# Kernel tuning notes

Hardware: AMD Instinct MI355X
Metric: run time of the kernel (lower is better)

The kernel has to match this reference:

```python
import jax, jax.numpy as jnp
import numpy as np
import math
from jax import lax

B, HID, HD, TD = 16384, 4096, 256, 64
IN_DIM = HID + 6 + TD
NL = 4
SOURCE_SCALE = 0.1


def hat(w):
    z = jnp.zeros_like(w[..., 0])
    wx, wy, wz = w[..., 0], w[..., 1], w[..., 2]
    return jnp.stack([
        jnp.stack([z, -wz, wy], -1),
        jnp.stack([wz, z, -wx], -1),
        jnp.stack([-wy, wx, z], -1)], -2)


def exp_se3(xi):
    # xi: [B,6] = (omega, v); returns [B,4,4]
    w, v = xi[:, :3], xi[:, 3:]
    th = jnp.sqrt(jnp.sum(w * w, -1) + 1e-20)[:, None, None]
    th2 = th * th
    small = th < 1e-3
    ths = jnp.where(small, 1.0, th)
    A = jnp.where(small, 1.0 - th2 / 6.0, jnp.sin(ths) / ths)
    Bc = jnp.where(small, 0.5 - th2 / 24.0, (1.0 - jnp.cos(ths)) / (ths * ths))
    Cc = jnp.where(small, 1.0 / 6.0 - th2 / 120.0, (ths - jnp.sin(ths)) / (ths ** 3))
    W = hat(w)
    W2 = W @ W
    I = jnp.eye(3, dtype=xi.dtype)
    R = I + A * W + Bc * W2
    V = I + Bc * W + Cc * W2
    t = jnp.einsum('bij,bj->bi', V, v)
    top = jnp.concatenate([R, t[:, :, None]], -1)
    bot = jnp.broadcast_to(jnp.array([0.0, 0.0, 0.0, 1.0], xi.dtype), (xi.shape[0], 1, 4))
    return jnp.concatenate([top, bot], -2)


def log_se3(X):
    # X: [B,4,4] -> xi: [B,6]
    R = X[:, :3, :3]
    p = X[:, :3, 3]
    tr = R[:, 0, 0] + R[:, 1, 1] + R[:, 2, 2]
    c = jnp.clip((tr - 1.0) * 0.5, -1.0 + 1e-7, 1.0 - 1e-7)
    th = jnp.arccos(c)[:, None, None]
    small = th < 1e-3
    ths = jnp.where(small, 1.0, th)
    fac = jnp.where(small, 0.5 + th * th / 12.0, ths / (2.0 * jnp.sin(ths)))
    wvee = jnp.stack([R[:, 2, 1] - R[:, 1, 2], R[:, 0, 2] - R[:, 2, 0], R[:, 1, 0] - R[:, 0, 1]], -1)
    w = fac[:, :, 0] * wvee
    W = hat(w)
    W2 = W @ W
    D = jnp.where(small, 1.0 / 12.0, (1.0 - ths * jnp.sin(ths) / (2.0 * (1.0 - jnp.cos(ths)))) / (ths * ths))
    I = jnp.eye(3, dtype=X.dtype)
    Vinv = I - 0.5 * W + D * W2
    v = jnp.einsum('bij,bj->bi', Vinv, p)
    return jnp.concatenate([w, v], -1)


def time_embed(t):
    # t: [B,1] -> [B,TD]
    half = TD // 2
    freqs = jnp.exp(jnp.arange(half, dtype=t.dtype) * (-math.log(10000.0) / (half - 1)))
    e = t * freqs[None, :]
    return jnp.concatenate([jnp.sin(e), jnp.cos(e)], -1)


def layernorm(x, g, b):
    m = jnp.mean(x, -1, keepdims=True)
    var = jnp.mean((x - m) ** 2, -1, keepdims=True)
    return (x - m) * lax.rsqrt(var + 1e-5) * g + b


def setup_inputs() -> dict:
    key = jax.random.key(0)
    ks = jax.random.split(key, 10)
    def lin(k, i, o):
        return jax.random.normal(k, (i, o), jnp.float32) / np.float32(np.sqrt(i))
    return {
        'h': jax.random.normal(ks[0], (B, HID), jnp.float32),
        'xi0': jax.random.normal(ks[1], (B, 6), jnp.float32),
        'W0': lin(ks[2], IN_DIM, HD),
        'b0': jnp.zeros((HD,), jnp.float32),
        'g0': jnp.ones((HD,), jnp.float32),
        'be0': jnp.zeros((HD,), jnp.float32),
        'Wr': jax.random.normal(ks[3], (NL - 1, HD, HD), jnp.float32) / np.float32(np.sqrt(HD)),
        'br': jnp.zeros((NL - 1, HD), jnp.float32),
        'gr': jnp.ones((NL - 1, HD), jnp.float32),
        'ber': jnp.zeros((NL - 1, HD), jnp.float32),
        'Wout': 0.05 * jax.random.normal(ks[4], (HD, 6), jnp.float32),
        'bout': jnp.zeros((6,), jnp.float32),
        'gW1': lin(ks[5], HID, 64),
        'gb1': jnp.zeros((64,), jnp.float32),
        'gW2': lin(ks[6], 64, 1),
        'gb2': jnp.zeros((1,), jnp.float32),
        'n_steps': 10,
    }


def reference(h, xi0, W0, b0, g0, be0, Wr, br, gr, ber, Wout, bout, gW1, gb1, gW2, gb2, n_steps):
    dt = 1.0 / n_steps
    X0 = exp_se3(SOURCE_SCALE * xi0)

    def mlp(x):
        y = layernorm(jax.nn.gelu(x @ W0 + b0, approximate=False), g0, be0)
        for i in range(Wr.shape[0]):
            y = layernorm(jax.nn.gelu(y @ Wr[i] + br[i], approximate=False), gr[i], ber[i])
        return y @ Wout + bout

    def step(X_t, tval):
        xi_t = log_se3(X_t)
        temb = time_embed(jnp.ones((X_t.shape[0], 1), X_t.dtype) * tval)
        v = mlp(jnp.concatenate([h, xi_t, temb], -1))
        X_next = jnp.einsum('bij,bjk->bik', X_t, exp_se3(dt * v))
        return X_next, None

    ts = jnp.arange(n_steps, dtype=h.dtype) * dt
    X1, _ = lax.scan(step, X0, ts)
    gripper = jax.nn.sigmoid(jax.nn.gelu(h @ gW1 + gb1, approximate=False) @ gW2 + gb2)
    return X1, gripper
```

## Files before the change

### kernel.cpp

```cpp
#include <hip/hip_runtime.h>
#include <math.h>

typedef __attribute__((ext_vector_type(8))) __bf16 bf16_8;
typedef __attribute__((ext_vector_type(4))) float f32x4;

#define WS_HPROJ 0
#define WS_BT    16777216
#define WS_WRT   19398656
#define WS_CT    19791872

__device__ __forceinline__ float gelu_f(float x) {
    return 0.5f * x * (1.0f + erff(0.70710678118654752440f * x));
}

__device__ __forceinline__ void exp_se3_dev(const float xi[6], float R[9], float t[3]) {
    float wx = xi[0], wy = xi[1], wz = xi[2];
    float vx = xi[3], vy = xi[4], vz = xi[5];
    float ww = wx*wx + wy*wy + wz*wz;
    float th2 = ww + 1e-20f;
    float th = sqrtf(th2);
    float A, Bc, Cc;
    if (th < 1e-3f) {
        A = 1.f - th2*(1.f/6.f);
        Bc = 0.5f - th2*(1.f/24.f);
        Cc = (1.f/6.f) - th2*(1.f/120.f);
    } else {
        float s = sinf(th), c = cosf(th);
        A = s/th;
        Bc = (1.f - c)/th2;
        Cc = (th - s)/(th2*th);
    }
    float W2[9] = { wx*wx - ww, wx*wy,       wx*wz,
                    wy*wx,      wy*wy - ww,  wy*wz,
                    wz*wx,      wz*wy,       wz*wz - ww };
    R[0] = 1.f + Bc*W2[0];  R[1] = -A*wz + Bc*W2[1]; R[2] =  A*wy + Bc*W2[2];
    R[3] =  A*wz + Bc*W2[3]; R[4] = 1.f + Bc*W2[4];  R[5] = -A*wx + Bc*W2[5];
    R[6] = -A*wy + Bc*W2[6]; R[7] =  A*wx + Bc*W2[7]; R[8] = 1.f + Bc*W2[8];
    float V[9];
    V[0] = 1.f + Cc*W2[0];   V[1] = -Bc*wz + Cc*W2[1]; V[2] =  Bc*wy + Cc*W2[2];
    V[3] =  Bc*wz + Cc*W2[3]; V[4] = 1.f + Cc*W2[4];   V[5] = -Bc*wx + Cc*W2[5];
    V[6] = -Bc*wy + Cc*W2[6]; V[7] =  Bc*wx + Cc*W2[7]; V[8] = 1.f + Cc*W2[8];
    t[0] = V[0]*vx + V[1]*vy + V[2]*vz;
    t[1] = V[3]*vx + V[4]*vy + V[5]*vz;
    t[2] = V[6]*vx + V[7]*vy + V[8]*vz;
}

__device__ __forceinline__ void log_se3_dev(const float R[9], const float p[3], float xi[6]) {
    float tr = R[0] + R[4] + R[8];
    float c = 0.5f*(tr - 1.f);
    c = fminf(fmaxf(c, -1.f + 1e-7f), 1.f - 1e-7f);
    float th = acosf(c);
    float fac, D;
    if (th < 1e-3f) {
        fac = 0.5f + th*th*(1.f/12.f);
        D = 1.f/12.f;
    } else {
        float s = sinf(th), co = cosf(th);
        fac = th/(2.f*s);
        D = (1.f - th*s/(2.f*(1.f - co)))/(th*th);
    }
    float wx = fac*(R[7] - R[5]);
    float wy = fac*(R[2] - R[6]);
    float wz = fac*(R[3] - R[1]);
    float ww = wx*wx + wy*wy + wz*wz;
    float W2[9] = { wx*wx - ww, wx*wy,       wx*wz,
                    wy*wx,      wy*wy - ww,  wy*wz,
                    wz*wx,      wz*wy,       wz*wz - ww };
    float Vi[9];
    Vi[0] = 1.f + D*W2[0];    Vi[1] =  0.5f*wz + D*W2[1]; Vi[2] = -0.5f*wy + D*W2[2];
    Vi[3] = -0.5f*wz + D*W2[3]; Vi[4] = 1.f + D*W2[4];    Vi[5] =  0.5f*wx + D*W2[5];
    Vi[6] =  0.5f*wy + D*W2[6]; Vi[7] = -0.5f*wx + D*W2[7]; Vi[8] = 1.f + D*W2[8];
    xi[0] = wx; xi[1] = wy; xi[2] = wz;
    xi[3] = Vi[0]*p[0] + Vi[1]*p[1] + Vi[2]*p[2];
    xi[4] = Vi[3]*p[0] + Vi[4]*p[1] + Vi[5]*p[2];
    xi[5] = Vi[6]*p[0] + Vi[7]*p[1] + Vi[8]*p[2];
}

__global__ void prep_frag(const float* __restrict__ W0, const float* __restrict__ gW1,
                          const float* __restrict__ Wr, __bf16* __restrict__ BT2,
                          __bf16* __restrict__ WrT2) {
    const int tid = threadIdx.x;
    const int l = tid & 63, q = l >> 4, ln = l & 15;
    if (blockIdx.x < 640) {
        const int t = blockIdx.x * 4 + (tid >> 6);
        const int s = t / 20, ntg = t % 20;
        const int col = ntg*16 + ln;
        const int kbase = s*32 + q*8;
        bf16_8 o;
        if (col < 256) {
            #pragma unroll
            for (int e = 0; e < 8; ++e) o[e] = (__bf16)W0[(size_t)(kbase+e)*256 + col];
        } else {
            #pragma unroll
            for (int e = 0; e < 8; ++e) o[e] = (__bf16)gW1[(size_t)(kbase+e)*64 + (col-256)];
        }
        *(bf16_8*)(BT2 + (size_t)t*512 + l*8) = o;
    } else {
        const int t2 = (blockIdx.x - 640) * 4 + (tid >> 6);
        const int L = t2 >> 7, rem = t2 & 127, sl = rem >> 4, ntg = rem & 15;
        const int col = ntg*16 + ln;
        const int kbase = sl*32 + q*8;
        bf16_8 o;
        #pragma unroll
        for (int e = 0; e < 8; ++e)
            o[e] = (__bf16)Wr[(size_t)L*65536 + (size_t)(kbase+e)*256 + col];
        *(bf16_8*)(WrT2 + (size_t)t2*512 + l*8) = o;
    }
}

__global__ void prep_ct(const float* __restrict__ W0, const float* __restrict__ b0,
                        const int* __restrict__ nsp, float* __restrict__ ct) {
    int s = blockIdx.x;
    int ns = *nsp;
    if (s >= ns) return;
    int col = threadIdx.x;
    float t = (float)s / (float)ns;
    float acc = b0[col];
    #pragma unroll
    for (int d = 0; d < 32; d++) {
        float f = expf((float)d * -0.29710775393471563f);
        float e = t * f;
        acc += sinf(e) * W0[(size_t)(4102 + d)*256 + col];
        acc += cosf(e) * W0[(size_t)(4134 + d)*256 + col];
    }
    ct[s*256 + col] = acc;
}

__device__ __forceinline__ void k2_loada(float4 (&A)[2][2][2], const float* hbase, int st) {
    #pragma unroll
    for (int mt = 0; mt < 2; ++mt)
        #pragma unroll
        for (int kk = 0; kk < 2; ++kk) {
            const float* p = hbase + (size_t)mt*16*4096 + st*64 + kk*32;
            A[mt][kk][0] = *(const float4*)p;
            A[mt][kk][1] = *(const float4*)(p + 4);
        }
}
__device__ __forceinline__ void k2_loadb(bf16_8 (&Bv)[2][5], const __bf16* bbase, int st) {
    #pragma unroll
    for (int kk = 0; kk < 2; ++kk)
        #pragma unroll
        for (int jn = 0; jn < 5; ++jn)
            Bv[kk][jn] = *(const bf16_8*)(bbase + (size_t)((st*2 + kk)*20 + jn*4)*512);
}
__device__ __forceinline__ void k2_mm(f32x4 (&acc)[2][5], const float4 (&A)[2][2][2],
                                      const bf16_8 (&Bv)[2][5]) {
    #pragma unroll
    for (int kk = 0; kk < 2; ++kk) {
        bf16_8 af[2];
        #pragma unroll
        for (int mt = 0; mt < 2; ++mt) {
            af[mt][0] = (__bf16)A[mt][kk][0].x; af[mt][1] = (__bf16)A[mt][kk][0].y;
            af[mt][2] = (__bf16)A[mt][kk][0].z; af[mt][3] = (__bf16)A[mt][kk][0].w;
            af[mt][4] = (__bf16)A[mt][kk][1].x; af[mt][5] = (__bf16)A[mt][kk][1].y;
            af[mt][6] = (__bf16)A[mt][kk][1].z; af[mt][7] = (__bf16)A[mt][kk][1].w;
        }
        #pragma unroll
        for (int mt = 0; mt < 2; ++mt)
            #pragma unroll
            for (int jn = 0; jn < 5; ++jn)
                acc[mt][jn] = __builtin_amdgcn_mfma_f32_16x16x32_bf16(af[mt], Bv[kk][jn], acc[mt][jn], 0, 0, 0);
    }
}

__launch_bounds__(256, 2)
__global__ void k2(const float* __restrict__ h, const __bf16* __restrict__ BT2,
                   const float* __restrict__ gb1, const float* __restrict__ gW2,
                   const float* __restrict__ gb2, float* __restrict__ hproj,
                   float* __restrict__ grip) {
    __shared__ float gpart[32][4];

    const int tid = threadIdx.x;
    const int w = tid >> 6;
    const int l = tid & 63;
    const int q = l >> 4;
    const int ln = l & 15;
    const int m0 = blockIdx.x * 32;

    const float*  hbase = h + (size_t)(m0 + ln)*4096 + q*8;
    const __bf16* bbase = BT2 + (size_t)w*512 + (size_t)l*8;

    f32x4 acc[2][5];
    const f32x4 zv = {0.f, 0.f, 0.f, 0.f};
    #pragma unroll
    for (int a = 0; a < 2; ++a)
        #pragma unroll
        for (int b = 0; b < 5; ++b) acc[a][b] = zv;

    float4 A0[2][2][2], A1[2][2][2];
    bf16_8 B0[2][5], B1[2][5];
    k2_loada(A0, hbase, 0); k2_loadb(B0, bbase, 0);
    for (int st = 0; st < 64; st += 2) {
        if ((st & 7) == 0 && st) __syncthreads();
        k2_loada(A1, hbase, st + 1); k2_loadb(B1, bbase, st + 1);
        k2_mm(acc, A0, B0);
        if (st < 62) { k2_loada(A0, hbase, st + 2); k2_loadb(B0, bbase, st + 2); }
        k2_mm(acc, A1, B1);
    }

    #pragma unroll
    for (int mt = 0; mt < 2; ++mt)
        #pragma unroll
        for (int jn = 0; jn < 4; ++jn) {
            int col = (w + jn*4)*16 + ln;
            #pragma unroll
            for (int r = 0; r < 4; ++r) {
                int row = mt*16 + q*4 + r;
                hproj[(size_t)(m0 + row)*256 + col] = acc[mt][jn][r];
            }
        }
    {
        int cg = w*16 + ln;
        float b1v = gb1[cg];
        float w2v = gW2[cg];
        float ps[2][4];
        #pragma unroll
        for (int mt = 0; mt < 2; ++mt)
            #pragma unroll
            for (int r = 0; r < 4; ++r)
                ps[mt][r] = gelu_f(acc[mt][4][r] + b1v) * w2v;
        #pragma unroll
        for (int off = 1; off < 16; off <<= 1)
            #pragma unroll
            for (int mt = 0; mt < 2; ++mt)
                #pragma unroll
                for (int r = 0; r < 4; ++r)
                    ps[mt][r] += __shfl_xor(ps[mt][r], off, 64);
        if (ln == 0)
            #pragma unroll
            for (int mt = 0; mt < 2; ++mt)
                #pragma unroll
                for (int r = 0; r < 4; ++r)
                    gpart[mt*16 + q*4 + r][w] = ps[mt][r];
    }
    __syncthreads();
    if (tid < 32) {
        float g = gpart[tid][0] + gpart[tid][1] + gpart[tid][2] + gpart[tid][3] + gb2[0];
        grip[m0 + tid] = 1.f / (1.f + expf(-g));
    }
}

__launch_bounds__(256, 2)
__global__ void k3(const float* __restrict__ hproj,
                   const __bf16* __restrict__ WrT2,
                   const float* __restrict__ ct,
                   const float* __restrict__ W0,
                   const float* __restrict__ Wout,
                   const float* __restrict__ bout,
                   const float* __restrict__ br,
                   const float* __restrict__ gr,
                   const float* __restrict__ ber,
                   const float* __restrict__ g0,
                   const float* __restrict__ be0,
                   const float* __restrict__ xi0,
                   const int* __restrict__ nsp,
                   float* __restrict__ out) {
    __shared__ __align__(16) __bf16 Ysh[32*264];
    __shared__ float xiL[32*6];
    __shared__ float rowred[32*16];
    __shared__ float vpart[32*8*6];
    __shared__ __align__(16) __bf16 woutT[6*256];
    __shared__ float Xsh[32][12];
    __shared__ float ctL[256];
    __shared__ __align__(16) __bf16 w0xiL[6*256];

    const int tid = threadIdx.x;
    const int w = tid >> 6;
    const int l = tid & 63;
    const int q = l >> 4;
    const int ln = l & 15;
    const int m0 = blockIdx.x * 32;
    const int ns = *nsp;
    const float dt = 1.0f / (float)ns;

    const int prow = tid >> 3;
    const int pcb  = (tid & 7) * 32;

    if (tid < 32) {
        float xi[6];
        #pragma unroll
        for (int j = 0; j < 6; ++j) xi[j] = 0.1f * xi0[(size_t)(m0 + tid)*6 + j];
        float R[9], tt[3];
        exp_se3_dev(xi, R, tt);
        #pragma unroll
        for (int j = 0; j < 9; ++j) Xsh[tid][j] = R[j];
        #pragma unroll
        for (int j = 0; j < 3; ++j) Xsh[tid][9+j] = tt[j];
    }
    for (int i = tid; i < 1536; i += 256) w0xiL[i] = (__bf16)W0[(size_t)4096*256 + i];
    for (int i = tid; i < 1536; i += 256) {
        int j = i >> 8, k = i & 255;
        woutT[i] = (__bf16)Wout[(size_t)k*6 + j];
    }
    __syncthreads();

    for (int s = 0; s < ns; ++s) {
        ctL[tid] = ct[s*256 + tid];
        if (tid < 32) {
            float R[9], p[3], xi[6];
            #pragma unroll
            for (int j = 0; j < 9; ++j) R[j] = Xsh[tid][j];
            #pragma unroll
            for (int j = 0; j < 3; ++j) p[j] = Xsh[tid][9+j];
            log_se3_dev(R, p, xi);
            #pragma unroll
            for (int j = 0; j < 6; ++j) xiL[tid*6 + j] = xi[j];
        }
        __syncthreads();

        float gv[32];
        {
            float xr[6];
            #pragma unroll
            for (int j = 0; j < 6; ++j) xr[j] = xiL[prow*6 + j];
            const float* hp = hproj + (size_t)(m0 + prow)*256 + pcb;
            #pragma unroll
            for (int c8 = 0; c8 < 4; ++c8) {
                float4 h0 = *(const float4*)(hp + c8*8);
                float4 h1 = *(const float4*)(hp + c8*8 + 4);
                float4 c0 = *(const float4*)(ctL + pcb + c8*8);
                float4 c1 = *(const float4*)(ctL + pcb + c8*8 + 4);
                float pr[8] = { h0.x + c0.x, h0.y + c0.y, h0.z + c0.z, h0.w + c0.w,
                                h1.x + c1.x, h1.y + c1.y, h1.z + c1.z, h1.w + c1.w };
                #pragma unroll
                for (int j = 0; j < 6; ++j) {
                    bf16_8 wv = *(const bf16_8*)(w0xiL + j*256 + pcb + c8*8);
                    #pragma unroll
                    for (int e = 0; e < 8; ++e) pr[e] += xr[j] * (float)wv[e];
                }
                #pragma unroll
                for (int e = 0; e < 8; ++e) gv[c8*8 + e] = gelu_f(pr[e]);
            }
            float ps = 0.f, pq = 0.f;
            #pragma unroll
            for (int c = 0; c < 32; ++c) { ps += gv[c]; pq += gv[c]*gv[c]; }
            rowred[prow*16 + (tid & 7)*2 + 0] = ps;
            rowred[prow*16 + (tid & 7)*2 + 1] = pq;
        }
        __syncthreads();
        if (tid < 32) {
            float sm = 0.f, sq = 0.f;
            #pragma unroll
            for (int k = 0; k < 8; ++k) { sm += rowred[tid*16 + k*2]; sq += rowred[tid*16 + k*2 + 1]; }
            float mean = sm * (1.f/256.f);
            float var  = sq * (1.f/256.f) - mean*mean;
            rowred[tid*16 + 0] = mean;
            rowred[tid*16 + 1] = rsqrtf(var + 1e-5f);
        }
        __syncthreads();
        {
            float mean = rowred[prow*16 + 0], rstd = rowred[prow*16 + 1];
            #pragma unroll
            for (int c8 = 0; c8 < 4; ++c8) {
                float4 ga = *(const float4*)(g0 + pcb + c8*8);
                float4 gb = *(const float4*)(g0 + pcb + c8*8 + 4);
                float4 ba = *(const float4*)(be0 + pcb + c8*8);
                float4 bb = *(const float4*)(be0 + pcb + c8*8 + 4);
                bf16_8 v8;
                v8[0] = (__bf16)((gv[c8*8+0] - mean)*rstd*ga.x + ba.x);
                v8[1] = (__bf16)((gv[c8*8+1] - mean)*rstd*ga.y + ba.y);
                v8[2] = (__bf16)((gv[c8*8+2] - mean)*rstd*ga.z + ba.z);
                v8[3] = (__bf16)((gv[c8*8+3] - mean)*rstd*ga.w + ba.w);
                v8[4] = (__bf16)((gv[c8*8+4] - mean)*rstd*gb.x + bb.x);
                v8[5] = (__bf16)((gv[c8*8+5] - mean)*rstd*gb.y + bb.y);
                v8[6] = (__bf16)((gv[c8*8+6] - mean)*rstd*gb.z + bb.z);
                v8[7] = (__bf16)((gv[c8*8+7] - mean)*rstd*gb.w + bb.w);
                *(bf16_8*)(Ysh + prow*264 + pcb + c8*8) = v8;
            }
        }
        __syncthreads();

        #pragma unroll 1
        for (int L = 0; L < 3; ++L) {
            f32x4 acc[2][4];
            const f32x4 zv = {0.f, 0.f, 0.f, 0.f};
            #pragma unroll
            for (int a = 0; a < 2; ++a)
                #pragma unroll
                for (int b = 0; b < 4; ++b) acc[a][b] = zv;
            const __bf16* wfrag = WrT2 + (size_t)L*128*512 + (size_t)l*8;
            #pragma unroll
            for (int sl = 0; sl < 8; ++sl) {
                bf16_8 af[2], bfv[4];
                #pragma unroll
                for (int mt = 0; mt < 2; ++mt)
                    af[mt] = *(const bf16_8*)(Ysh + (mt*16 + ln)*264 + sl*32 + q*8);
                #pragma unroll
                for (int nt = 0; nt < 4; ++nt)
                    bfv[nt] = *(const bf16_8*)(wfrag + (size_t)(sl*16 + w + nt*4)*512);
                #pragma unroll
                for (int mt = 0; mt < 2; ++mt)
                    #pragma unroll
                    for (int nt = 0; nt < 4; ++nt)
                        acc[mt][nt] = __builtin_amdgcn_mfma_f32_16x16x32_bf16(af[mt], bfv[nt], acc[mt][nt], 0, 0, 0);
            }
            const float* brL = br + L*256;
            const float* grL = gr + L*256;
            const float* beL = ber + L*256;
            float gelv[2][4][4];
            float ps[2][4], pq2[2][4];
            #pragma unroll
            for (int mt = 0; mt < 2; ++mt)
                #pragma unroll
                for (int r = 0; r < 4; ++r) { ps[mt][r] = 0.f; pq2[mt][r] = 0.f; }
            #pragma unroll
            for (int nt = 0; nt < 4; ++nt) {
                int col = (w + nt*4)*16 + ln;
                float bb = brL[col];
                #pragma unroll
                for (int mt = 0; mt < 2; ++mt)
                    #pragma unroll
                    for (int r = 0; r < 4; ++r) {
                        float u = gelu_f(acc[mt][nt][r] + bb);
                        gelv[mt][nt][r] = u;
                        ps[mt][r] += u;
                        pq2[mt][r] += u*u;
                    }
            }
            #pragma unroll
            for (int off = 1; off < 16; off <<= 1)
                #pragma unroll
                for (int mt = 0; mt < 2; ++mt)
                    #pragma unroll
                    for (int r = 0; r < 4; ++r) {
                        ps[mt][r]  += __shfl_xor(ps[mt][r],  off, 64);
                        pq2[mt][r] += __shfl_xor(pq2[mt][r], off, 64);
                    }
            if (ln == 0)
                #pragma unroll
                for (int mt = 0; mt < 2; ++mt)
                    #pragma unroll
                    for (int r = 0; r < 4; ++r) {
                        int row = mt*16 + q*4 + r;
                        rowred[row*16 + w*2 + 0] = ps[mt][r];
                        rowred[row*16 + w*2 + 1] = pq2[mt][r];
                    }
            __syncthreads();
            if (tid < 32) {
                float sm = 0.f, sq = 0.f;
                #pragma unroll
                for (int k = 0; k < 4; ++k) { sm += rowred[tid*16 + k*2]; sq += rowred[tid*16 + k*2 + 1]; }
                float mean = sm * (1.f/256.f);
                float var  = sq * (1.f/256.f) - mean*mean;
                rowred[tid*16 + 0] = mean;
                rowred[tid*16 + 1] = rsqrtf(var + 1e-5f);
            }
            __syncthreads();
            #pragma unroll
            for (int nt = 0; nt < 4; ++nt) {
                int col = (w + nt*4)*16 + ln;
                float gg = grL[col], bb2 = beL[col];
                #pragma unroll
                for (int mt = 0; mt < 2; ++mt)
                    #pragma unroll
                    for (int r = 0; r < 4; ++r) {
                        int row = mt*16 + q*4 + r;
                        float mean = rowred[row*16 + 0];
                        float rstd = rowred[row*16 + 1];
                        Ysh[row*264 + col] = (__bf16)((gelv[mt][nt][r] - mean)*rstd*gg + bb2);
                    }
            }
            __syncthreads();
        }

        {
            float p6[6] = {0.f, 0.f, 0.f, 0.f, 0.f, 0.f};
            const int kb = (tid & 7) * 32;
            #pragma unroll
            for (int kc = 0; kc < 4; ++kc) {
                bf16_8 yv = *(const bf16_8*)(Ysh + prow*264 + kb + kc*8);
                float yf[8];
                #pragma unroll
                for (int e = 0; e < 8; ++e) yf[e] = (float)yv[e];
                #pragma unroll
                for (int j = 0; j < 6; ++j) {
                    bf16_8 wv = *(const bf16_8*)(woutT + j*256 + kb + kc*8);
                    #pragma unroll
                    for (int e = 0; e < 8; ++e) p6[j] += yf[e] * (float)wv[e];
                }
            }
            #pragma unroll
            for (int j = 0; j < 6; ++j) vpart[(prow*8 + (tid & 7))*6 + j] = p6[j];
        }
        __syncthreads();
        if (tid < 32) {
            float v6[6];
            #pragma unroll
            for (int j = 0; j < 6; ++j) {
                float sv = 0.f;
                #pragma unroll
                for (int c = 0; c < 8; ++c) sv += vpart[(tid*8 + c)*6 + j];
                v6[j] = dt * (sv + bout[j]);
            }
            float Re[9], te[3];
            exp_se3_dev(v6, Re, te);
            float R0[9], t0[3];
            #pragma unroll
            for (int j = 0; j < 9; ++j) R0[j] = Xsh[tid][j];
            #pragma unroll
            for (int j = 0; j < 3; ++j) t0[j] = Xsh[tid][9+j];
            float Rn[9], tn[3];
            #pragma unroll
            for (int i = 0; i < 3; ++i)
                #pragma unroll
                for (int j2 = 0; j2 < 3; ++j2)
                    Rn[i*3+j2] = R0[i*3+0]*Re[0*3+j2] + R0[i*3+1]*Re[1*3+j2] + R0[i*3+2]*Re[2*3+j2];
            #pragma unroll
            for (int i = 0; i < 3; ++i)
                tn[i] = R0[i*3+0]*te[0] + R0[i*3+1]*te[1] + R0[i*3+2]*te[2] + t0[i];
            #pragma unroll
            for (int j = 0; j < 9; ++j) Xsh[tid][j] = Rn[j];
            #pragma unroll
            for (int j = 0; j < 3; ++j) Xsh[tid][9+j] = tn[j];
            if (s == ns - 1) {
                float* o = out + (size_t)(m0 + tid)*16;
                o[0]  = Rn[0]; o[1]  = Rn[1]; o[2]  = Rn[2]; o[3]  = tn[0];
                o[4]  = Rn[3]; o[5]  = Rn[4]; o[6]  = Rn[5]; o[7]  = tn[1];
                o[8]  = Rn[6]; o[9]  = Rn[7]; o[10] = Rn[8]; o[11] = tn[2];
                o[12] = 0.f; o[13] = 0.f; o[14] = 0.f; o[15] = 1.f;
            }
        }
        __syncthreads();
    }
}

extern "C" void kernel_launch(void* const* d_in, const int* in_sizes, int n_in,
                              void* d_out, int out_size, void* d_ws, size_t ws_size,
                              hipStream_t stream) {
    const float* h    = (const float*)d_in[0];
    const float* xi0  = (const float*)d_in[1];
    const float* W0   = (const float*)d_in[2];
    const float* b0   = (const float*)d_in[3];
    const float* g0   = (const float*)d_in[4];
    const float* be0  = (const float*)d_in[5];
    const float* Wr   = (const float*)d_in[6];
    const float* br   = (const float*)d_in[7];
    const float* gr   = (const float*)d_in[8];
    const float* ber  = (const float*)d_in[9];
    const float* Wout = (const float*)d_in[10];
    const float* bout = (const float*)d_in[11];
    const float* gW1  = (const float*)d_in[12];
    const float* gb1  = (const float*)d_in[13];
    const float* gW2  = (const float*)d_in[14];
    const float* gb2  = (const float*)d_in[15];
    const int*   nsp  = (const int*)d_in[16];
    float* out = (float*)d_out;

    char* ws = (char*)d_ws;
    float*  hproj = (float*)(ws + WS_HPROJ);
    __bf16* BT2   = (__bf16*)(ws + WS_BT);
    __bf16* WrT2  = (__bf16*)(ws + WS_WRT);
    float*  ct    = (float*)(ws + WS_CT);

    prep_frag<<<736, 256, 0, stream>>>(W0, gW1, Wr, BT2, WrT2);
    prep_ct<<<16, 256, 0, stream>>>(W0, b0, nsp, ct);
    k2<<<512, 256, 0, stream>>>(h, BT2, gb1, gW2, gb2, hproj, out + (size_t)16384*16);
    k3<<<512, 256, 0, stream>>>(hproj, WrT2, ct, W0, Wout, bout, br, gr, ber, g0, be0, xi0, nsp, out);
}
```

Baseline: 857.2 us.

## Stage h tiles through double-buffered LDS in bf16 for the k2 projection GEMM

Previously every wave in the k2 block read the full 32-row fp32 A tile of h straight from global memory, so each row was fetched four times per block. Now each thread loads one 8-element slice with nontemporal loads, converts it to bf16 and writes it to one of two padded LDS buffers. All waves then read A fragments from LDS, with barriers alternating between the two buffers. This cuts redundant global traffic for h and the repeated conversion work, at the cost of a barrier per k-step and extra LDS use.

```diff
diff --git a/kernel.cpp b/kernel.cpp
--- a/kernel.cpp
+++ b/kernel.cpp
@@ -126,35 +126,30 @@
     ct[s*256 + col] = acc;
 }
 
-__device__ __forceinline__ void k2_loada(float4 (&A)[2][2][2], const float* hbase, int st) {
-    #pragma unroll
-    for (int mt = 0; mt < 2; ++mt)
-        #pragma unroll
-        for (int kk = 0; kk < 2; ++kk) {
-            const float* p = hbase + (size_t)mt*16*4096 + st*64 + kk*32;
-            A[mt][kk][0] = *(const float4*)p;
-            A[mt][kk][1] = *(const float4*)(p + 4);
-        }
-}
-__device__ __forceinline__ void k2_loadb(bf16_8 (&Bv)[2][5], const __bf16* bbase, int st) {
+__device__ __forceinline__ void k2_issueA(f32x4 (&P)[2], const float* hrow, int st) {
+    P[0] = __builtin_nontemporal_load((const f32x4*)(hrow + st*64));
+    P[1] = __builtin_nontemporal_load((const f32x4*)(hrow + st*64 + 4));
+}
+__device__ __forceinline__ void k2_writeA(__bf16* dst, const f32x4 (&P)[2]) {
+    bf16_8 v;
+    v[0]=(__bf16)P[0][0]; v[1]=(__bf16)P[0][1]; v[2]=(__bf16)P[0][2]; v[3]=(__bf16)P[0][3];
+    v[4]=(__bf16)P[1][0]; v[5]=(__bf16)P[1][1]; v[6]=(__bf16)P[1][2]; v[7]=(__bf16)P[1][3];
+    *(bf16_8*)dst = v;
+}
+__device__ __forceinline__ void k2_issueB(bf16_8 (&Bv)[2][5], const __bf16* bbase, int st) {
     #pragma unroll
     for (int kk = 0; kk < 2; ++kk)
         #pragma unroll
         for (int jn = 0; jn < 5; ++jn)
             Bv[kk][jn] = *(const bf16_8*)(bbase + (size_t)((st*2 + kk)*20 + jn*4)*512);
 }
-__device__ __forceinline__ void k2_mm(f32x4 (&acc)[2][5], const float4 (&A)[2][2][2],
-                                      const bf16_8 (&Bv)[2][5]) {
+__device__ __forceinline__ void k2_mm2(f32x4 (&acc)[2][5], const __bf16* Ab, int ln, int q,
+                                       const bf16_8 (&Bv)[2][5]) {
     #pragma unroll
     for (int kk = 0; kk < 2; ++kk) {
         bf16_8 af[2];
-        #pragma unroll
-        for (int mt = 0; mt < 2; ++mt) {
-            af[mt][0] = (__bf16)A[mt][kk][0].x; af[mt][1] = (__bf16)A[mt][kk][0].y;
-            af[mt][2] = (__bf16)A[mt][kk][0].z; af[mt][3] = (__bf16)A[mt][kk][0].w;
-            af[mt][4] = (__bf16)A[mt][kk][1].x; af[mt][5] = (__bf16)A[mt][kk][1].y;
-            af[mt][6] = (__bf16)A[mt][kk][1].z; af[mt][7] = (__bf16)A[mt][kk][1].w;
-        }
+        af[0] = *(const bf16_8*)(Ab + (0*16 + ln)*72 + kk*32 + q*8);
+        af[1] = *(const bf16_8*)(Ab + (1*16 + ln)*72 + kk*32 + q*8);
         #pragma unroll
         for (int mt = 0; mt < 2; ++mt)
             #pragma unroll
@@ -168,6 +163,8 @@
                    const float* __restrict__ gb1, const float* __restrict__ gW2,
                    const float* __restrict__ gb2, float* __restrict__ hproj,
                    float* __restrict__ grip) {
+    __shared__ __align__(16) __bf16 Abuf0[32*72];
+    __shared__ __align__(16) __bf16 Abuf1[32*72];
     __shared__ float gpart[32][4];
 
     const int tid = threadIdx.x;
@@ -177,7 +174,12 @@
     const int ln = l & 15;
     const int m0 = blockIdx.x * 32;
 
-    const float*  hbase = h + (size_t)(m0 + ln)*4096 + q*8;
+    const int r  = tid >> 3;
+    const int c0 = (tid & 7) * 8;
+    const float* hrow = h + (size_t)(m0 + r)*4096 + c0;
+    __bf16* aw0 = Abuf0 + r*72 + c0;
+    __bf16* aw1 = Abuf1 + r*72 + c0;
+
     const __bf16* bbase = BT2 + (size_t)w*512 + (size_t)l*8;
 
     f32x4 acc[2][5];
@@ -187,15 +189,35 @@
         #pragma unroll
         for (int b = 0; b < 5; ++b) acc[a][b] = zv;
 
-    float4 A0[2][2][2], A1[2][2][2];
+    f32x4 PA[2], PB[2];
     bf16_8 B0[2][5], B1[2][5];
-    k2_loada(A0, hbase, 0); k2_loadb(B0, bbase, 0);
-    for (int st = 0; st < 64; st += 2) {
-        if ((st & 7) == 0 && st) __syncthreads();
-        k2_loada(A1, hbase, st + 1); k2_loadb(B1, bbase, st + 1);
-        k2_mm(acc, A0, B0);
-        if (st < 62) { k2_loada(A0, hbase, st + 2); k2_loadb(B0, bbase, st + 2); }
-        k2_mm(acc, A1, B1);
+
+    k2_issueA(PA, hrow, 0);
+    k2_issueB(B0, bbase, 0);
+    k2_issueA(PB, hrow, 1);
+    k2_issueB(B1, bbase, 1);
+    k2_writeA(aw0, PA);
+    k2_issueA(PA, hrow, 2);
+    asm volatile("s_waitcnt lgkmcnt(0)" ::: "memory");
+    __builtin_amdgcn_s_barrier();
+
+    #pragma unroll 1
+    for (int t = 0; t < 32; ++t) {
+        const int st = 2*t;
+        k2_mm2(acc, Abuf0, ln, q, B0);
+        k2_writeA(aw1, PB);
+        if (st + 3 < 64) k2_issueA(PB, hrow, st + 3);
+        if (st + 2 < 64) k2_issueB(B0, bbase, st + 2);
+        asm volatile("s_waitcnt lgkmcnt(0)" ::: "memory");
+        __builtin_amdgcn_s_barrier();
+        k2_mm2(acc, Abuf1, ln, q, B1);
+        if (st + 2 < 64) {
+            k2_writeA(aw0, PA);
+            if (st + 4 < 64) k2_issueA(PA, hrow, st + 4);
+            if (st + 3 < 64) k2_issueB(B1, bbase, st + 3);
+            asm volatile("s_waitcnt lgkmcnt(0)" ::: "memory");
+            __builtin_amdgcn_s_barrier();
+        }
     }
 
     #pragma unroll
@@ -204,9 +226,9 @@
         for (int jn = 0; jn < 4; ++jn) {
             int col = (w + jn*4)*16 + ln;
             #pragma unroll
-            for (int r = 0; r < 4; ++r) {
-                int row = mt*16 + q*4 + r;
-                hproj[(size_t)(m0 + row)*256 + col] = acc[mt][jn][r];
+            for (int r2 = 0; r2 < 4; ++r2) {
+                int row = mt*16 + q*4 + r2;
+                hproj[(size_t)(m0 + row)*256 + col] = acc[mt][jn][r2];
             }
         }
     {
@@ -217,21 +239,21 @@
         #pragma unroll
         for (int mt = 0; mt < 2; ++mt)
             #pragma unroll
-            for (int r = 0; r < 4; ++r)
-                ps[mt][r] = gelu_f(acc[mt][4][r] + b1v) * w2v;
+            for (int r2 = 0; r2 < 4; ++r2)
+                ps[mt][r2] = gelu_f(acc[mt][4][r2] + b1v) * w2v;
         #pragma unroll
         for (int off = 1; off < 16; off <<= 1)
             #pragma unroll
             for (int mt = 0; mt < 2; ++mt)
                 #pragma unroll
-                for (int r = 0; r < 4; ++r)
-                    ps[mt][r] += __shfl_xor(ps[mt][r], off, 64);
+                for (int r2 = 0; r2 < 4; ++r2)
+                    ps[mt][r2] += __shfl_xor(ps[mt][r2], off, 64);
         if (ln == 0)
             #pragma unroll
             for (int mt = 0; mt < 2; ++mt)
                 #pragma unroll
-                for (int r = 0; r < 4; ++r)
-                    gpart[mt*16 + q*4 + r][w] = ps[mt][r];
+                for (int r2 = 0; r2 < 4; ++r2)
+                    gpart[mt*16 + q*4 + r2][w] = ps[mt][r2];
     }
     __syncthreads();
     if (tid < 32) {
```

Result: faster. 779.1 us (-9.1%).
